# Kernel tuning notes

Hardware: AMD Instinct MI355X
Metric: run time of the kernel (lower is better)

The kernel has to match this reference:

```python
import jax, jax.numpy as jnp
import numpy as np

B, S, H = 2, 2048, 1024
NH, DH = 16, 64  # num heads, head dim

def setup_inputs() -> dict:
    key = jax.random.key(0)
    ks = jax.random.split(key, 4)
    scale = 0.02
    return {
        "hidden_states": jax.random.normal(ks[0], (B, S, H), dtype=jnp.float32),
        "attention_mask": jnp.zeros((B, 1, 1, S), dtype=jnp.float32),  # additive mask
        "Wq": jax.random.normal(ks[1], (H, H), dtype=jnp.float32) * scale,
        "bq": jnp.zeros((H,), dtype=jnp.float32),
        "Wk": jax.random.normal(ks[2], (H, H), dtype=jnp.float32) * scale,
        "bk": jnp.zeros((H,), dtype=jnp.float32),
        "Wv": jax.random.normal(ks[3], (H, H), dtype=jnp.float32) * scale,
        "bv": jnp.zeros((H,), dtype=jnp.float32),
    }

def _split_heads(x):
    # [B,S,H] -> [B,NH,S,DH]
    return x.reshape(B, S, NH, DH).transpose(0, 2, 1, 3)

def reference(hidden_states, attention_mask, Wq, bq, Wk, bk, Wv, bv):
    q = _split_heads(hidden_states @ Wq + bq)
    k = _split_heads(hidden_states @ Wk + bk)
    v = _split_heads(hidden_states @ Wv + bv)
    # scores: [B,NH,S,S]
    scores = jnp.einsum('bhqd,bhkd->bhqk', q, k) / jnp.asarray(np.sqrt(DH), scores_dtype := q.dtype)
    scores = scores + attention_mask  # additive mask broadcast
    probs = jax.nn.softmax(scores, axis=-1)
    out = jnp.einsum('bhqk,bhkd->bhqd', probs, v)  # [B,NH,S,DH]
    out = out.transpose(0, 2, 1, 3).reshape(B, S, H)
    return out
```

## Files before the change

### kernel.cpp

```cpp
#include <hip/hip_runtime.h>
#include <hip/hip_bf16.h>

#define Bn  2
#define Sn  2048
#define Hn  1024
#define NHn 16
#define DHn 64
#define Mn  (Bn * Sn)

typedef __attribute__((ext_vector_type(4)))  float    f32x4;
typedef __attribute__((ext_vector_type(16))) float    f32x16;
typedef __attribute__((ext_vector_type(8)))  _Float16 h8;
typedef __attribute__((ext_vector_type(4)))  _Float16 h4;

#define MFMA16F(a, b, c) __builtin_amdgcn_mfma_f32_16x16x32_f16(a, b, c, 0, 0, 0)
#define MFMA32F(a, b, c) __builtin_amdgcn_mfma_f32_32x32x16_f16(a, b, c, 0, 0, 0)

__device__ __forceinline__ void glds16(const void* g, void* l) {
    __builtin_amdgcn_global_load_lds(
        (const __attribute__((address_space(1))) unsigned int*)g,
        (__attribute__((address_space(3))) unsigned int*)l, 16, 0, 0);
}

__global__ __launch_bounds__(256) void cvt_x(
    const float* __restrict__ X, _Float16* __restrict__ Xh)
{
    const int i = blockIdx.x * 256 + threadIdx.x;
    float4 x = ((const float4*)X)[i];
    h4 o;
    o[0] = (_Float16)x.x; o[1] = (_Float16)x.y;
    o[2] = (_Float16)x.z; o[3] = (_Float16)x.w;
    *(h4*)&Xh[(size_t)i * 4] = o;
}

__global__ __launch_bounds__(256) void cvt_wT(
    const float* __restrict__ W0, const float* __restrict__ W1,
    const float* __restrict__ W2, _Float16* __restrict__ WT)
{
    const int which = blockIdx.z;
    const float* W = (which == 0) ? W0 : (which == 1 ? W1 : W2);
    _Float16* O = WT + (size_t)which * Hn * Hn;

    const int k0 = blockIdx.x * 64;
    const int n0 = blockIdx.y * 64;
    const int tid = threadIdx.x;

    __shared__ float Ws[64][65];

#pragma unroll
    for (int it = 0; it < 4; ++it) {
        const int idx = tid + 256 * it;
        const int row = idx >> 4, c4 = (idx & 15) * 4;
        float4 w = *(const float4*)&W[(size_t)(k0 + row) * Hn + n0 + c4];
        Ws[row][c4 + 0] = w.x; Ws[row][c4 + 1] = w.y;
        Ws[row][c4 + 2] = w.z; Ws[row][c4 + 3] = w.w;
    }
    __syncthreads();
#pragma unroll
    for (int it = 0; it < 16; ++it) {
        const int e = tid + 256 * it;
        const int k = e & 63, n = e >> 6;
        O[(size_t)(n0 + n) * Hn + k0 + k] = (_Float16)Ws[k][n];
    }
}

__global__ __launch_bounds__(256) void qkv_mfma(
    const _Float16* __restrict__ Xh, const _Float16* __restrict__ WTA,
    const float* __restrict__ b0, const float* __restrict__ b1,
    const float* __restrict__ b2,
    _Float16* __restrict__ Qh, _Float16* __restrict__ Kh,
    _Float16* __restrict__ VTh)
{
    const int which = blockIdx.z;
    const _Float16* WT = WTA + (size_t)which * Hn * Hn;
    const float* bias = (which == 0) ? b0 : (which == 1 ? b1 : b2);
    _Float16* Dst = (which == 0) ? Qh : (which == 1 ? Kh : VTh);

    const int m0 = blockIdx.x * 128;
    const int n0 = blockIdx.y * 128;
    const int tid  = threadIdx.x;
    const int wid  = tid >> 6;
    const int lane = tid & 63;
    const int l16  = lane & 15;
    const int quad = lane >> 4;
    const int wm = wid >> 1, wn = wid & 1;

    __shared__ _Float16 Ah[128 * 32], Bh[128 * 32];

    f32x4 acc[4][4];
#pragma unroll
    for (int i = 0; i < 4; ++i)
#pragma unroll
        for (int j = 0; j < 4; ++j) acc[i][j] = (f32x4){0.f, 0.f, 0.f, 0.f};

    for (int kt = 0; kt < Hn / 32; ++kt) {
        const int k0 = kt * 32;
        __syncthreads();
#pragma unroll
        for (int c = 0; c < 2; ++c) {
            const int idx = (wid * 2 + c) * 64 + lane;
            const int row = idx >> 2;
            const int cg  = (idx & 3) ^ (row & 3);
            glds16(&Xh[(size_t)(m0 + row) * Hn + k0 + cg * 8],
                   &Ah[(wid * 2 + c) * 512]);
            glds16(&WT[(size_t)(n0 + row) * Hn + k0 + cg * 8],
                   &Bh[(wid * 2 + c) * 512]);
        }
        __syncthreads();

        h8 xa[4], wb[4];
#pragma unroll
        for (int t = 0; t < 4; ++t) {
            const int ar = wm * 64 + t * 16 + l16;
            const int br = wn * 64 + t * 16 + l16;
            xa[t] = *(const h8*)&Ah[ar * 32 + ((quad ^ (ar & 3)) * 8)];
            wb[t] = *(const h8*)&Bh[br * 32 + ((quad ^ (br & 3)) * 8)];
        }
        if (which < 2) {
#pragma unroll
            for (int i = 0; i < 4; ++i)
#pragma unroll
                for (int j = 0; j < 4; ++j)
                    acc[i][j] = MFMA16F(xa[i], wb[j], acc[i][j]);
        } else {
#pragma unroll
            for (int i = 0; i < 4; ++i)
#pragma unroll
                for (int j = 0; j < 4; ++j)
                    acc[i][j] = MFMA16F(wb[i], xa[j], acc[i][j]);
        }
    }

    if (which < 2) {
#pragma unroll
        for (int j = 0; j < 4; ++j) {
            const int n = n0 + wn * 64 + j * 16 + l16;
            const float bv = bias[n];
            const int hh = n >> 6, dd = n & 63;
#pragma unroll
            for (int i = 0; i < 4; ++i) {
                const int mb = m0 + wm * 64 + i * 16 + quad * 4;
#pragma unroll
                for (int r = 0; r < 4; ++r) {
                    const int m = mb + r;
                    const int b = m >> 11, s = m & (Sn - 1);
                    Dst[(((size_t)b * NHn + hh) * Sn + s) * DHn + dd] =
                        (_Float16)(acc[i][j][r] + bv);
                }
            }
        }
    } else {
#pragma unroll
        for (int i = 0; i < 4; ++i) {
#pragma unroll
            for (int r = 0; r < 4; ++r) {
                const int n = n0 + wn * 64 + i * 16 + quad * 4 + r;
                const float bv = bias[n];
                const int hh = n >> 6, dd = n & 63;
#pragma unroll
                for (int j = 0; j < 4; ++j) {
                    const int m = m0 + wm * 64 + j * 16 + l16;
                    const int b = m >> 11, s = m & (Sn - 1);
                    Dst[(((size_t)b * NHn + hh) * DHn + dd) * Sn + s] =
                        (_Float16)(acc[i][j][r] + bv);
                }
            }
        }
    }
}

__global__ __launch_bounds__(256) void attn(
    const _Float16* __restrict__ Qh, const _Float16* __restrict__ Kh,
    const _Float16* __restrict__ VTh, const float* __restrict__ mask,
    float* __restrict__ Out)
{
    const int qb = blockIdx.x;
    const int h  = blockIdx.y;
    const int b  = blockIdx.z;
    const int bh = b * NHn + h;

    const int tid  = threadIdx.x;
    const int wid  = tid >> 6;
    const int lane = tid & 63;
    const int l32  = lane & 31;
    const int hi   = lane >> 5;

    __shared__ _Float16 Kb[2][4096];
    __shared__ _Float16 Vb[2][4096];
    __shared__ _Float16 Pws[4][32 * 72];
    __shared__ float Mlds[2][64];
    __shared__ float Ilds[4][32];

    const int q0 = qb * 128 + wid * 32;
    const size_t qbase = ((size_t)bh * Sn + q0 + l32) * DHn;
    h8 qf[4];
#pragma unroll
    for (int kd = 0; kd < 4; ++kd)
        qf[kd] = *(const h8*)&Qh[qbase + kd * 16 + hi * 8];

    f32x16 o[2];
#pragma unroll
    for (int dt = 0; dt < 2; ++dt) o[dt] = (f32x16)(0.f);
    float l_lane = 0.f;

    const _Float16* Kg = Kh  + (size_t)bh * Sn * DHn;
    const _Float16* Vg = VTh + (size_t)bh * DHn * Sn;

#pragma unroll
    for (int c = 0; c < 2; ++c) {
        const int idx = (wid * 2 + c) * 64 + lane;
        const int row = idx >> 3;
        const int cg  = (idx & 7) ^ (row & 7);
        glds16(&Kg[(size_t)row * DHn + cg * 8], &Kb[0][(wid * 2 + c) * 512]);
        glds16(&Vg[(size_t)row * Sn  + cg * 8], &Vb[0][(wid * 2 + c) * 512]);
    }
    if (tid < 64) Mlds[0][tid] = mask[(size_t)b * Sn + tid];

    for (int kt = 0; kt < Sn / 64; ++kt) {
        const int cur = kt & 1;
        __syncthreads();

        if (kt + 1 < Sn / 64) {
            const int nxt = cur ^ 1;
            const int koff = (kt + 1) * 64;
#pragma unroll
            for (int c = 0; c < 2; ++c) {
                const int idx = (wid * 2 + c) * 64 + lane;
                const int row = idx >> 3;
                const int cg  = (idx & 7) ^ (row & 7);
                glds16(&Kg[(size_t)(koff + row) * DHn + cg * 8],
                       &Kb[nxt][(wid * 2 + c) * 512]);
                glds16(&Vg[(size_t)row * Sn + koff + cg * 8],
                       &Vb[nxt][(wid * 2 + c) * 512]);
            }
            if (tid < 64) Mlds[nxt][tid] = mask[(size_t)b * Sn + koff + tid];
        }

        f32x16 s[2];
#pragma unroll
        for (int t = 0; t < 2; ++t) {
            f32x16 c = (f32x16)(0.f);
#pragma unroll
            for (int kd = 0; kd < 4; ++kd) {
                const int row = t * 32 + l32;
                h8 kf = *(const h8*)&Kb[cur][row * 64 +
                                             (((kd * 2 + hi) ^ (row & 7)) * 8)];
                c = MFMA32F(kf, qf[kd], c);
            }
            s[t] = c;
        }

#pragma unroll
        for (int t = 0; t < 2; ++t) {
#pragma unroll
            for (int g2 = 0; g2 < 4; ++g2) {
                float4 mv = *(const float4*)&Mlds[cur][t * 32 + hi * 4 + g2 * 8];
                h4 pk;
#pragma unroll
                for (int e = 0; e < 4; ++e) {
                    const float p = __expf(s[t][g2 * 4 + e] * 0.125f +
                                           ((const float*)&mv)[e]);
                    l_lane += p;
                    pk[e] = (_Float16)p;
                }
                *(h4*)&Pws[wid][l32 * 72 + t * 32 + hi * 4 + g2 * 8] = pk;
            }
        }

#pragma unroll
        for (int ks = 0; ks < 4; ++ks) {
            h8 pa = *(const h8*)&Pws[wid][l32 * 72 + ks * 16 + hi * 8];
#pragma unroll
            for (int dt = 0; dt < 2; ++dt) {
                const int row = dt * 32 + l32;
                h8 vf = *(const h8*)&Vb[cur][row * 64 +
                                             (((ks * 2 + hi) ^ (row & 7)) * 8)];
                o[dt] = MFMA32F(pa, vf, o[dt]);
            }
        }
    }

    const float l_tot = l_lane + __shfl_xor(l_lane, 32);
    if (lane < 32) Ilds[wid][l32] = 1.0f / l_tot;

#pragma unroll
    for (int g2 = 0; g2 < 4; ++g2) {
        float4 iv = *(const float4*)&Ilds[wid][hi * 4 + g2 * 8];
#pragma unroll
        for (int e = 0; e < 4; ++e) {
            const int r = g2 * 4 + e;
            const int q = q0 + 4 * hi + 8 * g2 + e;
            const size_t ob = ((size_t)b * Sn + q) * Hn + h * DHn;
            const float sc = ((const float*)&iv)[e];
#pragma unroll
            for (int dt = 0; dt < 2; ++dt)
                Out[ob + dt * 32 + l32] = o[dt][r] * sc;
        }
    }
}

extern "C" void kernel_launch(void* const* d_in, const int* in_sizes, int n_in,
                              void* d_out, int out_size, void* d_ws, size_t ws_size,
                              hipStream_t stream) {
    const float* X    = (const float*)d_in[0];
    const float* mask = (const float*)d_in[1];
    const float* Wq   = (const float*)d_in[2];
    const float* bq   = (const float*)d_in[3];
    const float* Wk   = (const float*)d_in[4];
    const float* bk   = (const float*)d_in[5];
    const float* Wv   = (const float*)d_in[6];
    const float* bv   = (const float*)d_in[7];
    float* out = (float*)d_out;

    const size_t NE = (size_t)Mn * Hn;
    _Float16* Xh  = (_Float16*)d_ws;
    _Float16* WT  = Xh + NE;
    _Float16* Qh  = WT + (size_t)3 * Hn * Hn;
    _Float16* Kh  = Qh + NE;
    _Float16* VTh = Kh + NE;

    cvt_x<<<dim3(Mn * Hn / 1024), dim3(256), 0, stream>>>(X, Xh);
    cvt_wT<<<dim3(16, 16, 3), dim3(256), 0, stream>>>(Wq, Wk, Wv, WT);

    dim3 g1(Mn / 128, Hn / 128, 3), b1(256);
    qkv_mfma<<<g1, b1, 0, stream>>>(Xh, WT, bq, bk, bv, Qh, Kh, VTh);

    dim3 g2(Sn / 128, NHn, Bn), b2(256);
    attn<<<g2, b2, 0, stream>>>(Qh, Kh, VTh, mask, out);
}
```

Baseline: 191.5 us.

## Keep attention probabilities in registers and use exp2 with pre-scaled mask

The attention inner loop no longer round-trips P through shared memory. Probabilities are packed to fp16 with cvt_pkrtz and exchanged between wave halves via cross-lane shuffles to form the MFMA A operand directly. The softmax uses hardware exp2 with scale*log2e folded in, and a new small kernel pre-multiplies the mask by log2e so it is read from global memory instead of staged in LDS. Pointer arithmetic for the K/V prefetch is also strength-reduced. This removes LDS traffic and some VALU work in exchange for an extra launch, shuffle overhead, and round-toward-zero fp16 conversion.

```diff
diff --git a/kernel.cpp b/kernel.cpp
--- a/kernel.cpp
+++ b/kernel.cpp
@@ -12,6 +12,7 @@
 typedef __attribute__((ext_vector_type(16))) float    f32x16;
 typedef __attribute__((ext_vector_type(8)))  _Float16 h8;
 typedef __attribute__((ext_vector_type(4)))  _Float16 h4;
+typedef __attribute__((ext_vector_type(2)))  __fp16   fp16v2;
 
 #define MFMA16F(a, b, c) __builtin_amdgcn_mfma_f32_16x16x32_f16(a, b, c, 0, 0, 0)
 #define MFMA32F(a, b, c) __builtin_amdgcn_mfma_f32_32x32x16_f16(a, b, c, 0, 0, 0)
@@ -20,6 +21,12 @@
     __builtin_amdgcn_global_load_lds(
         (const __attribute__((address_space(1))) unsigned int*)g,
         (__attribute__((address_space(3))) unsigned int*)l, 16, 0, 0);
+}
+
+__device__ __forceinline__ unsigned pkrtz(float a, float b) {
+    union { fp16v2 h; unsigned u; } c;
+    c.h = __builtin_amdgcn_cvt_pkrtz(a, b);
+    return c.u;
 }
 
 __global__ __launch_bounds__(256) void cvt_x(
@@ -31,6 +38,13 @@
     o[0] = (_Float16)x.x; o[1] = (_Float16)x.y;
     o[2] = (_Float16)x.z; o[3] = (_Float16)x.w;
     *(h4*)&Xh[(size_t)i * 4] = o;
+}
+
+__global__ __launch_bounds__(256) void cvt_mask(
+    const float* __restrict__ mask, float* __restrict__ mask2)
+{
+    const int i = blockIdx.x * 256 + threadIdx.x;
+    mask2[i] = mask[i] * 1.44269504f;
 }
 
 __global__ __launch_bounds__(256) void cvt_wT(
@@ -169,9 +183,11 @@
     }
 }
 
+#define SCALE_LOG2E 0.180336880f
+
 __global__ __launch_bounds__(256) void attn(
     const _Float16* __restrict__ Qh, const _Float16* __restrict__ Kh,
-    const _Float16* __restrict__ VTh, const float* __restrict__ mask,
+    const _Float16* __restrict__ VTh, const float* __restrict__ mask2,
     float* __restrict__ Out)
 {
     const int qb = blockIdx.x;
@@ -187,8 +203,6 @@
 
     __shared__ _Float16 Kb[2][4096];
     __shared__ _Float16 Vb[2][4096];
-    __shared__ _Float16 Pws[4][32 * 72];
-    __shared__ float Mlds[2][64];
     __shared__ float Ilds[4][32];
 
     const int q0 = qb * 128 + wid * 32;
@@ -203,81 +217,87 @@
     for (int dt = 0; dt < 2; ++dt) o[dt] = (f32x16)(0.f);
     float l_lane = 0.f;
 
-    const _Float16* Kg = Kh  + (size_t)bh * Sn * DHn;
-    const _Float16* Vg = VTh + (size_t)bh * DHn * Sn;
-
-#pragma unroll
-    for (int c = 0; c < 2; ++c) {
-        const int idx = (wid * 2 + c) * 64 + lane;
-        const int row = idx >> 3;
-        const int cg  = (idx & 7) ^ (row & 7);
-        glds16(&Kg[(size_t)row * DHn + cg * 8], &Kb[0][(wid * 2 + c) * 512]);
-        glds16(&Vg[(size_t)row * Sn  + cg * 8], &Vb[0][(wid * 2 + c) * 512]);
-    }
-    if (tid < 64) Mlds[0][tid] = mask[(size_t)b * Sn + tid];
+    const int idx0 = (wid * 2 + 0) * 64 + lane;
+    const int idx1 = (wid * 2 + 1) * 64 + lane;
+    const int row0 = idx0 >> 3, cg0 = (idx0 & 7) ^ (row0 & 7);
+    const int row1 = idx1 >> 3, cg1 = (idx1 & 7) ^ (row1 & 7);
+    const _Float16* kp0 = Kh  + (size_t)bh * Sn * DHn + (size_t)row0 * DHn + cg0 * 8;
+    const _Float16* kp1 = Kh  + (size_t)bh * Sn * DHn + (size_t)row1 * DHn + cg1 * 8;
+    const _Float16* vp0 = VTh + (size_t)bh * DHn * Sn + (size_t)row0 * Sn + cg0 * 8;
+    const _Float16* vp1 = VTh + (size_t)bh * DHn * Sn + (size_t)row1 * Sn + cg1 * 8;
+    _Float16* KbP = &Kb[0][0];
+    _Float16* VbP = &Vb[0][0];
+    const int ld0 = (wid * 2 + 0) * 512;
+    const int ld1 = (wid * 2 + 1) * 512;
+
+    const float* mp = mask2 + (size_t)b * Sn + hi * 4;
+
+    glds16(kp0, KbP + ld0);  glds16(kp1, KbP + ld1);
+    glds16(vp0, VbP + ld0);  glds16(vp1, VbP + ld1);
+    kp0 += 64 * DHn; kp1 += 64 * DHn; vp0 += 64; vp1 += 64;
 
     for (int kt = 0; kt < Sn / 64; ++kt) {
         const int cur = kt & 1;
         __syncthreads();
 
         if (kt + 1 < Sn / 64) {
-            const int nxt = cur ^ 1;
-            const int koff = (kt + 1) * 64;
-#pragma unroll
-            for (int c = 0; c < 2; ++c) {
-                const int idx = (wid * 2 + c) * 64 + lane;
-                const int row = idx >> 3;
-                const int cg  = (idx & 7) ^ (row & 7);
-                glds16(&Kg[(size_t)(koff + row) * DHn + cg * 8],
-                       &Kb[nxt][(wid * 2 + c) * 512]);
-                glds16(&Vg[(size_t)row * Sn + koff + cg * 8],
-                       &Vb[nxt][(wid * 2 + c) * 512]);
-            }
-            if (tid < 64) Mlds[nxt][tid] = mask[(size_t)b * Sn + koff + tid];
-        }
-
-        f32x16 s[2];
+            const int nb = (cur ^ 1) * 4096;
+            glds16(kp0, KbP + nb + ld0);  glds16(kp1, KbP + nb + ld1);
+            glds16(vp0, VbP + nb + ld0);  glds16(vp1, VbP + nb + ld1);
+            kp0 += 64 * DHn; kp1 += 64 * DHn; vp0 += 64; vp1 += 64;
+        }
+        const _Float16* Kc = KbP + cur * 4096;
+        const _Float16* Vc = VbP + cur * 4096;
+
 #pragma unroll
         for (int t = 0; t < 2; ++t) {
-            f32x16 c = (f32x16)(0.f);
+            f32x16 s = (f32x16)(0.f);
 #pragma unroll
             for (int kd = 0; kd < 4; ++kd) {
                 const int row = t * 32 + l32;
-                h8 kf = *(const h8*)&Kb[cur][row * 64 +
-                                             (((kd * 2 + hi) ^ (row & 7)) * 8)];
-                c = MFMA32F(kf, qf[kd], c);
-            }
-            s[t] = c;
-        }
-
-#pragma unroll
-        for (int t = 0; t < 2; ++t) {
+                h8 kf = *(const h8*)&Kc[row * 64 + (((kd * 2 + hi) ^ (row & 7)) * 8)];
+                s = MFMA32F(kf, qf[kd], s);
+            }
+
+            unsigned pk[4][2];
 #pragma unroll
             for (int g2 = 0; g2 < 4; ++g2) {
-                float4 mv = *(const float4*)&Mlds[cur][t * 32 + hi * 4 + g2 * 8];
-                h4 pk;
-#pragma unroll
-                for (int e = 0; e < 4; ++e) {
-                    const float p = __expf(s[t][g2 * 4 + e] * 0.125f +
-                                           ((const float*)&mv)[e]);
-                    l_lane += p;
-                    pk[e] = (_Float16)p;
-                }
-                *(h4*)&Pws[wid][l32 * 72 + t * 32 + hi * 4 + g2 * 8] = pk;
-            }
-        }
-
-#pragma unroll
-        for (int ks = 0; ks < 4; ++ks) {
-            h8 pa = *(const h8*)&Pws[wid][l32 * 72 + ks * 16 + hi * 8];
+                float4 mv = *(const float4*)&mp[t * 32 + g2 * 8];
+                float p0 = __builtin_amdgcn_exp2f(s[g2 * 4 + 0] * SCALE_LOG2E + mv.x);
+                float p1 = __builtin_amdgcn_exp2f(s[g2 * 4 + 1] * SCALE_LOG2E + mv.y);
+                float p2 = __builtin_amdgcn_exp2f(s[g2 * 4 + 2] * SCALE_LOG2E + mv.z);
+                float p3 = __builtin_amdgcn_exp2f(s[g2 * 4 + 3] * SCALE_LOG2E + mv.w);
+                l_lane += (p0 + p1) + (p2 + p3);
+                pk[g2][0] = pkrtz(p0, p1);
+                pk[g2][1] = pkrtz(p2, p3);
+            }
+
+            unsigned sx = hi ? pk[0][0] : pk[1][0];
+            unsigned sy = hi ? pk[0][1] : pk[1][1];
+            unsigned rx = __shfl_xor(sx, 32);
+            unsigned ry = __shfl_xor(sy, 32);
+            union { unsigned u[4]; h8 v; } af0;
+            if (hi == 0) { af0.u[0] = pk[0][0]; af0.u[1] = pk[0][1]; af0.u[2] = rx; af0.u[3] = ry; }
+            else         { af0.u[0] = rx;       af0.u[1] = ry;       af0.u[2] = pk[1][0]; af0.u[3] = pk[1][1]; }
+
+            unsigned sx2 = hi ? pk[2][0] : pk[3][0];
+            unsigned sy2 = hi ? pk[2][1] : pk[3][1];
+            unsigned rx2 = __shfl_xor(sx2, 32);
+            unsigned ry2 = __shfl_xor(sy2, 32);
+            union { unsigned u[4]; h8 v; } af1;
+            if (hi == 0) { af1.u[0] = pk[2][0]; af1.u[1] = pk[2][1]; af1.u[2] = rx2; af1.u[3] = ry2; }
+            else         { af1.u[0] = rx2;      af1.u[1] = ry2;      af1.u[2] = pk[3][0]; af1.u[3] = pk[3][1]; }
+
 #pragma unroll
             for (int dt = 0; dt < 2; ++dt) {
                 const int row = dt * 32 + l32;
-                h8 vf = *(const h8*)&Vb[cur][row * 64 +
-                                             (((ks * 2 + hi) ^ (row & 7)) * 8)];
-                o[dt] = MFMA32F(pa, vf, o[dt]);
-            }
-        }
+                h8 vf0 = *(const h8*)&Vc[row * 64 + (((t * 4 + hi)     ^ (row & 7)) * 8)];
+                o[dt] = MFMA32F(af0.v, vf0, o[dt]);
+                h8 vf1 = *(const h8*)&Vc[row * 64 + (((t * 4 + 2 + hi) ^ (row & 7)) * 8)];
+                o[dt] = MFMA32F(af1.v, vf1, o[dt]);
+            }
+        }
+        mp += 64;
     }
 
     const float l_tot = l_lane + __shfl_xor(l_lane, 32);
@@ -318,13 +338,15 @@
     _Float16* Qh  = WT + (size_t)3 * Hn * Hn;
     _Float16* Kh  = Qh + NE;
     _Float16* VTh = Kh + NE;
+    float*    m2  = (float*)(VTh + NE);
 
     cvt_x<<<dim3(Mn * Hn / 1024), dim3(256), 0, stream>>>(X, Xh);
+    cvt_mask<<<dim3(Bn * Sn / 256), dim3(256), 0, stream>>>(mask, m2);
     cvt_wT<<<dim3(16, 16, 3), dim3(256), 0, stream>>>(Wq, Wk, Wv, WT);
 
     dim3 g1(Mn / 128, Hn / 128, 3), b1(256);
     qkv_mfma<<<g1, b1, 0, stream>>>(Xh, WT, bq, bk, bv, Qh, Kh, VTh);
 
     dim3 g2(Sn / 128, NHn, Bn), b2(256);
-    attn<<<g2, b2, 0, stream>>>(Qh, Kh, VTh, mask, out);
-}
+    attn<<<g2, b2, 0, stream>>>(Qh, Kh, VTh, m2, out);
+}
```

Measured after the change: 218.3 us. 13.9% more time.
